# Performance work log

Hardware: AMD Instinct MI355X
Metric: run time of the kernel (lower is better)

The kernel has to match this reference:

```python
import jax, jax.numpy as jnp
import numpy as np

TEMPERATURE = 0.07


def setup_inputs() -> dict:
    key = jax.random.key(0)
    k1, k2 = jax.random.split(key)
    B, D = 4096, 512
    emb1 = jax.random.normal(k1, (B, D), dtype=jnp.float32)
    emb2 = jax.random.normal(k2, (B, D), dtype=jnp.float32)
    # module assumes L2-normalised embeddings
    emb1 = emb1 / jnp.linalg.norm(emb1, axis=-1, keepdims=True)
    emb2 = emb2 / jnp.linalg.norm(emb2, axis=-1, keepdims=True)
    return {"emb1": emb1, "emb2": emb2}


def reference(emb1, emb2):
    B = emb1.shape[0]
    emb = jnp.concatenate([emb1, emb2], axis=0)            # (2B, D)
    sim = jnp.einsum('id,jd->ij', emb, emb) / TEMPERATURE  # (2B, 2B)
    neg_inf = jnp.finfo(sim.dtype).min
    self_mask = jnp.eye(2 * B, dtype=bool)
    sim = jnp.where(self_mask, neg_inf, sim)
    labels = jnp.concatenate([jnp.arange(B, 2 * B), jnp.arange(B)])
    logp = jax.nn.log_softmax(sim, axis=-1)                # stable softmax CE
    nll = -jnp.take_along_axis(logp, labels[:, None], axis=-1)[:, 0]
    return jnp.mean(nll)
```

## Files before the change

kernel.cpp:

```cpp
#include <hip/hip_runtime.h>
#include <hip/hip_bf16.h>

#define B_    4096
#define D_    512
#define TB_   8192
#define BM    128
#define BK    128
#define NK    4
#define NTILE 64
#define NTRI  2080
#define INV_T 14.285714285714286f
#define SCL   (INV_T / 16129.0f)

typedef __attribute__((ext_vector_type(4))) int v4i;

#define GLOAD_LDS16(gp, lp)                                                        \
  __builtin_amdgcn_global_load_lds((const __attribute__((address_space(1))) void*)(gp), \
                                   (__attribute__((address_space(3))) void*)(lp),  \
                                   16, 0, 0)

__global__ void ntx_prep(const float* __restrict__ a, const float* __restrict__ b,
                         char* __restrict__ E8) {
  int t = blockIdx.x * blockDim.x + threadIdx.x;
  int i = t * 16;
  const float* src = (i < B_ * D_) ? (a + i) : (b + (i - B_ * D_));
  v4i o;
#pragma unroll
  for (int g = 0; g < 4; ++g) {
    float4 v = ((const float4*)src)[g];
    int q0 = __float2int_rn(v.x * 127.0f) & 255;
    int q1 = __float2int_rn(v.y * 127.0f) & 255;
    int q2 = __float2int_rn(v.z * 127.0f) & 255;
    int q3 = __float2int_rn(v.w * 127.0f) & 255;
    o[g] = q0 | (q1 << 8) | (q2 << 16) | (q3 << 24);
  }
  ((v4i*)E8)[t] = o;
}

__global__ __launch_bounds__(256, 2)
void ntx_sim(const char* __restrict__ E8, float* __restrict__ P,
             float* __restrict__ pos) {
  __shared__ __align__(16) char As[BM * BK];
  __shared__ __align__(16) char Bs[BM * BK];

  const int bid = blockIdx.x;
  const int t   = (bid & 7) * (NTRI / 8) + (bid >> 3);
  int ti = (int)((129.0f - sqrtf(16641.0f - 8.0f * (float)t)) * 0.5f);
  while (ti * (129 - ti) / 2 > t) --ti;
  while ((ti + 1) * (128 - ti) / 2 <= t) ++ti;
  const int tj = ti + (t - ti * (129 - ti) / 2);
  const int rowTile = ti * BM, colTile = tj * BM;
  const bool diag = (ti == tj);
  const bool posT = (tj == ti + B_ / BM);

  const int tid = threadIdx.x, lane = tid & 63, wave = tid >> 6;
  const int wr = wave >> 1, wc = wave & 1;
  const int llo = lane & 15, lhi = lane >> 4;

  unsigned offA[4], offB[4], ldsOf[4];
#pragma unroll
  for (int r = 0; r < 4; ++r) {
    int ch = r * 256 + tid, row = ch >> 3;
    int sc = ((ch & 7) ^ (row & 7)) << 4;
    offA[r]  = (unsigned)(rowTile + row) * D_ + sc;
    offB[r]  = (unsigned)(colTile + row) * D_ + sc;
    ldsOf[r] = (unsigned)ch * 16;
  }
  unsigned fA[2][4], fB[2][4];
#pragma unroll
  for (int ks = 0; ks < 2; ++ks)
#pragma unroll
    for (int m = 0; m < 4; ++m) {
      int chc = ks * 4 + lhi;
      int ra  = wr * 64 + m * 16 + llo;
      fA[ks][m] = (unsigned)(ra * BK + (((unsigned)chc ^ (ra & 7)) << 4));
      int rb  = wc * 64 + m * 16 + llo;
      fB[ks][m] = (unsigned)(rb * BK + (((unsigned)chc ^ (rb & 7)) << 4));
    }

  v4i acc[4][4] = {};

  for (int kt = 0; kt < NK; ++kt) {
    const unsigned kb = (unsigned)kt * BK;
#pragma unroll
    for (int r = 0; r < 4; ++r) GLOAD_LDS16(E8 + offA[r] + kb, &As[ldsOf[r]]);
#pragma unroll
    for (int r = 0; r < 4; ++r) GLOAD_LDS16(E8 + offB[r] + kb, &Bs[ldsOf[r]]);
    __syncthreads();
#pragma unroll
    for (int ks = 0; ks < 2; ++ks) {
      v4i af[4], bf[4];
#pragma unroll
      for (int m = 0; m < 4; ++m) {
        af[m] = *(const v4i*)&As[fA[ks][m]];
        bf[m] = *(const v4i*)&Bs[fB[ks][m]];
      }
#pragma unroll
      for (int m = 0; m < 4; ++m)
#pragma unroll
        for (int n = 0; n < 4; ++n)
          acc[m][n] = __builtin_amdgcn_mfma_i32_16x16x64_i8(af[m], bf[n],
                                                            acc[m][n], 0, 0, 0);
    }
    __syncthreads();
  }

  float* __restrict__ Prow = P + ((size_t)ti * 2 * NTILE + (size_t)tj * 2 + wc) * BM;
  float* __restrict__ Pcol = P + ((size_t)tj * 2 * NTILE + (size_t)ti * 2 + wr) * BM;
  float cs[4] = {0.f, 0.f, 0.f, 0.f};
#pragma unroll
  for (int m = 0; m < 4; ++m) {
    float rs[4] = {0.f, 0.f, 0.f, 0.f};
#pragma unroll
    for (int n = 0; n < 4; ++n) {
      int gc = colTile + wc * 64 + n * 16 + llo;
#pragma unroll
      for (int jj = 0; jj < 4; ++jj) {
        int gr = rowTile + wr * 64 + m * 16 + lhi * 4 + jj;
        float s = (float)acc[m][n][jj] * SCL;
        if (posT && gc - gr == B_) pos[gr] = s;
        float e = __expf(s);
        e = (diag && gr == gc) ? 0.0f : e;
        rs[jj] += e;
        cs[n]  += e;
      }
    }
#pragma unroll
    for (int jj = 0; jj < 4; ++jj) {
      float v = rs[jj];
      v += __shfl_xor(v, 1);
      v += __shfl_xor(v, 2);
      v += __shfl_xor(v, 4);
      v += __shfl_xor(v, 8);
      if (llo == 0) Prow[wr * 64 + m * 16 + lhi * 4 + jj] = v;
    }
  }
  if (diag) {
    ;
  } else {
#pragma unroll
    for (int n = 0; n < 4; ++n) {
      float v = cs[n];
      v += __shfl_xor(v, 16);
      v += __shfl_xor(v, 32);
      if (lhi == 0) Pcol[wc * 64 + n * 16 + llo] = v;
    }
  }
}

__global__ void ntx_fin1(const float* __restrict__ P, const float* __restrict__ pos,
                         float* __restrict__ par) {
  int r = blockIdx.x * 256 + threadIdx.x;
  int ti = r >> 7, rloc = r & 127;
  const float* base = P + (size_t)ti * 2 * NTILE * BM + rloc;
  float s = 0.f;
#pragma unroll 16
  for (int j = 0; j < 2 * NTILE; ++j) s += base[j * BM];
  float nll = __logf(s) - pos[r & (B_ - 1)];
  float v = nll;
#pragma unroll
  for (int off = 1; off < 64; off <<= 1) v += __shfl_xor(v, off);
  __shared__ float sm[4];
  if ((threadIdx.x & 63) == 0) sm[threadIdx.x >> 6] = v;
  __syncthreads();
  if (threadIdx.x == 0) par[blockIdx.x] = sm[0] + sm[1] + sm[2] + sm[3];
}

__global__ void ntx_fin2(const float* __restrict__ par, float* __restrict__ out) {
  int t = threadIdx.x;
  float s = (t < 32) ? par[t] : 0.f;
#pragma unroll
  for (int off = 1; off < 32; off <<= 1) s += __shfl_xor(s, off);
  if (t == 0) out[0] = s * (1.0f / TB_);
}

extern "C" void kernel_launch(void* const* d_in, const int* in_sizes, int n_in,
                              void* d_out, int out_size, void* d_ws, size_t ws_size,
                              hipStream_t stream) {
  const float* e1 = (const float*)d_in[0];
  const float* e2 = (const float*)d_in[1];
  float* out = (float*)d_out;
  char*  E8  = (char*)d_ws;
  float* P   = (float*)((char*)d_ws + (size_t)TB_ * D_);
  float* pos = P + (size_t)NTILE * 2 * NTILE * BM;
  float* par = pos + B_;

  ntx_prep<<<1024, 256, 0, stream>>>(e1, e2, E8);
  ntx_sim<<<NTRI, 256, 0, stream>>>(E8, P, pos);
  ntx_fin1<<<TB_ / 256, 256, 0, stream>>>(P, pos, par);
  ntx_fin2<<<1, 64, 0, stream>>>(par, out);
}
```

Before: 50.27 us.

## Use 1024-thread blocks with 4x4 waves and LDS-reduced tile partial sums

Grows the similarity kernel from 4 to 16 waves per 128x128 tile, so each wave computes a 32x32 sub-tile and each thread issues one global-to-LDS load per operand per k-step. Row and column exp-sums are reduced across waves in shared memory before a single write per tile, which halves the partial-sum buffer and the number of entries fin1 has to sum. exp is rewritten as exp2 with a prescaled constant. The trade is less register-level data reuse per wave (fewer MFMAs per LDS fragment read), an extra block barrier, and the requirement that 1024-thread blocks can reach the requested occupancy.

After: 58.39 us. 1.16x slower.

```diff
diff --git a/kernel.cpp b/kernel.cpp
--- a/kernel.cpp
+++ b/kernel.cpp
@@ -11,6 +11,7 @@
 #define NTRI  2080
 #define INV_T 14.285714285714286f
 #define SCL   (INV_T / 16129.0f)
+#define SCL2  (SCL * 1.4426950408889634f)
 
 typedef __attribute__((ext_vector_type(4))) int v4i;
 
@@ -37,7 +38,7 @@
   ((v4i*)E8)[t] = o;
 }
 
-__global__ __launch_bounds__(256, 2)
+__global__ __launch_bounds__(1024, 4)
 void ntx_sim(const char* __restrict__ E8, float* __restrict__ P,
              float* __restrict__ pos) {
   __shared__ __align__(16) char As[BM * BK];
@@ -54,72 +55,68 @@
   const bool posT = (tj == ti + B_ / BM);
 
   const int tid = threadIdx.x, lane = tid & 63, wave = tid >> 6;
-  const int wr = wave >> 1, wc = wave & 1;
+  const int wr = wave >> 2;
+  const int wc = wave & 3;
   const int llo = lane & 15, lhi = lane >> 4;
 
-  unsigned offA[4], offB[4], ldsOf[4];
-#pragma unroll
-  for (int r = 0; r < 4; ++r) {
-    int ch = r * 256 + tid, row = ch >> 3;
-    int sc = ((ch & 7) ^ (row & 7)) << 4;
-    offA[r]  = (unsigned)(rowTile + row) * D_ + sc;
-    offB[r]  = (unsigned)(colTile + row) * D_ + sc;
-    ldsOf[r] = (unsigned)ch * 16;
-  }
-  unsigned fA[2][4], fB[2][4];
+  const int ch = tid, srow = ch >> 3;
+  const int sc = ((ch & 7) ^ (srow & 7)) << 4;
+  const unsigned offA  = (unsigned)(rowTile + srow) * D_ + sc;
+  const unsigned offB  = (unsigned)(colTile + srow) * D_ + sc;
+  const unsigned ldsOf = (unsigned)ch * 16;
+
+  unsigned fA[2][2], fB[2][2];
 #pragma unroll
   for (int ks = 0; ks < 2; ++ks)
 #pragma unroll
-    for (int m = 0; m < 4; ++m) {
+    for (int m = 0; m < 2; ++m) {
       int chc = ks * 4 + lhi;
-      int ra  = wr * 64 + m * 16 + llo;
+      int ra  = wr * 32 + m * 16 + llo;
       fA[ks][m] = (unsigned)(ra * BK + (((unsigned)chc ^ (ra & 7)) << 4));
-      int rb  = wc * 64 + m * 16 + llo;
+      int rb  = wc * 32 + m * 16 + llo;
       fB[ks][m] = (unsigned)(rb * BK + (((unsigned)chc ^ (rb & 7)) << 4));
     }
 
-  v4i acc[4][4] = {};
+  v4i acc[2][2] = {};
 
   for (int kt = 0; kt < NK; ++kt) {
     const unsigned kb = (unsigned)kt * BK;
-#pragma unroll
-    for (int r = 0; r < 4; ++r) GLOAD_LDS16(E8 + offA[r] + kb, &As[ldsOf[r]]);
-#pragma unroll
-    for (int r = 0; r < 4; ++r) GLOAD_LDS16(E8 + offB[r] + kb, &Bs[ldsOf[r]]);
+    GLOAD_LDS16(E8 + offA + kb, &As[ldsOf]);
+    GLOAD_LDS16(E8 + offB + kb, &Bs[ldsOf]);
     __syncthreads();
 #pragma unroll
     for (int ks = 0; ks < 2; ++ks) {
-      v4i af[4], bf[4];
+      v4i af[2], bf[2];
 #pragma unroll
-      for (int m = 0; m < 4; ++m) {
+      for (int m = 0; m < 2; ++m) {
         af[m] = *(const v4i*)&As[fA[ks][m]];
         bf[m] = *(const v4i*)&Bs[fB[ks][m]];
       }
 #pragma unroll
-      for (int m = 0; m < 4; ++m)
+      for (int m = 0; m < 2; ++m)
 #pragma unroll
-        for (int n = 0; n < 4; ++n)
+        for (int n = 0; n < 2; ++n)
           acc[m][n] = __builtin_amdgcn_mfma_i32_16x16x64_i8(af[m], bf[n],
                                                             acc[m][n], 0, 0, 0);
     }
     __syncthreads();
   }
 
-  float* __restrict__ Prow = P + ((size_t)ti * 2 * NTILE + (size_t)tj * 2 + wc) * BM;
-  float* __restrict__ Pcol = P + ((size_t)tj * 2 * NTILE + (size_t)ti * 2 + wr) * BM;
-  float cs[4] = {0.f, 0.f, 0.f, 0.f};
+  float* Rbuf = (float*)As;
+  float* Cbuf = (float*)Bs;
+  float cs[2] = {0.f, 0.f};
 #pragma unroll
-  for (int m = 0; m < 4; ++m) {
+  for (int m = 0; m < 2; ++m) {
     float rs[4] = {0.f, 0.f, 0.f, 0.f};
 #pragma unroll
-    for (int n = 0; n < 4; ++n) {
-      int gc = colTile + wc * 64 + n * 16 + llo;
+    for (int n = 0; n < 2; ++n) {
+      int gc = colTile + wc * 32 + n * 16 + llo;
 #pragma unroll
       for (int jj = 0; jj < 4; ++jj) {
-        int gr = rowTile + wr * 64 + m * 16 + lhi * 4 + jj;
-        float s = (float)acc[m][n][jj] * SCL;
-        if (posT && gc - gr == B_) pos[gr] = s;
-        float e = __expf(s);
+        int gr = rowTile + wr * 32 + m * 16 + lhi * 4 + jj;
+        float si = (float)acc[m][n][jj];
+        if (posT && gc - gr == B_) pos[gr] = si * SCL;
+        float e = exp2f(si * SCL2);
         e = (diag && gr == gc) ? 0.0f : e;
         rs[jj] += e;
         cs[n]  += e;
@@ -132,18 +129,25 @@
       v += __shfl_xor(v, 2);
       v += __shfl_xor(v, 4);
       v += __shfl_xor(v, 8);
-      if (llo == 0) Prow[wr * 64 + m * 16 + lhi * 4 + jj] = v;
+      if (llo == 0) Rbuf[wc * 128 + wr * 32 + m * 16 + lhi * 4 + jj] = v;
     }
   }
-  if (diag) {
-    ;
-  } else {
 #pragma unroll
-    for (int n = 0; n < 4; ++n) {
-      float v = cs[n];
-      v += __shfl_xor(v, 16);
-      v += __shfl_xor(v, 32);
-      if (lhi == 0) Pcol[wc * 64 + n * 16 + llo] = v;
+  for (int n = 0; n < 2; ++n) {
+    float v = cs[n];
+    v += __shfl_xor(v, 16);
+    v += __shfl_xor(v, 32);
+    if (lhi == 0) Cbuf[wr * 128 + wc * 32 + n * 16 + llo] = v;
+  }
+  __syncthreads();
+  if (tid < 128) {
+    float v = Rbuf[tid] + Rbuf[128 + tid] + Rbuf[256 + tid] + Rbuf[384 + tid];
+    P[((size_t)ti * NTILE + tj) * BM + tid] = v;
+  } else if (tid < 256) {
+    if (!diag) {
+      int c = tid - 128;
+      float v = Cbuf[c] + Cbuf[128 + c] + Cbuf[256 + c] + Cbuf[384 + c];
+      P[((size_t)tj * NTILE + ti) * BM + c] = v;
     }
   }
 }
@@ -152,10 +156,10 @@
                          float* __restrict__ par) {
   int r = blockIdx.x * 256 + threadIdx.x;
   int ti = r >> 7, rloc = r & 127;
-  const float* base = P + (size_t)ti * 2 * NTILE * BM + rloc;
+  const float* base = P + (size_t)ti * NTILE * BM + rloc;
   float s = 0.f;
 #pragma unroll 16
-  for (int j = 0; j < 2 * NTILE; ++j) s += base[j * BM];
+  for (int j = 0; j < NTILE; ++j) s += base[j * BM];
   float nll = __logf(s) - pos[r & (B_ - 1)];
   float v = nll;
 #pragma unroll
@@ -182,11 +186,11 @@
   float* out = (float*)d_out;
   char*  E8  = (char*)d_ws;
   float* P   = (float*)((char*)d_ws + (size_t)TB_ * D_);
-  float* pos = P + (size_t)NTILE * 2 * NTILE * BM;
+  float* pos = P + (size_t)NTILE * NTILE * BM;
   float* par = pos + B_;
 
   ntx_prep<<<1024, 256, 0, stream>>>(e1, e2, E8);
-  ntx_sim<<<NTRI, 256, 0, stream>>>(E8, P, pos);
+  ntx_sim<<<NTRI, 1024, 0, stream>>>(E8, P, pos);
   ntx_fin1<<<TB_ / 256, 256, 0, stream>>>(P, pos, par);
   ntx_fin2<<<1, 64, 0, stream>>>(par, out);
 }
```

## Enlarge similarity tiles to 256 with 1024-thread blocks and LDS partial-sum reduction

Applied to the files above, without the earlier changes.

Doubles the output tile of the int8 similarity GEMM to 256x256, with 16 waves per block. This halves the global reloads of each embedding row and cuts the number of triangle blocks. Row and column exp-sums are combined across waves in LDS before one write per tile, which shrinks the partial-sum buffer the finisher must scan. Risks: far fewer blocks (528) for load balance, and the launch bound of 1024 threads with 4 blocks may force a very tight VGPR budget and spill the 64-register accumulators.

Result: slower. 55.25 us (+9.9%).

```diff
diff --git a/kernel.cpp b/kernel.cpp
--- a/kernel.cpp
+++ b/kernel.cpp
@@ -4,11 +4,11 @@
 #define B_    4096
 #define D_    512
 #define TB_   8192
-#define BM    128
+#define BM    256
 #define BK    128
 #define NK    4
-#define NTILE 64
-#define NTRI  2080
+#define NT    32
+#define NTRI  528
 #define INV_T 14.285714285714286f
 #define SCL   (INV_T / 16129.0f)
 
@@ -37,7 +37,7 @@
   ((v4i*)E8)[t] = o;
 }
 
-__global__ __launch_bounds__(256, 2)
+__global__ __launch_bounds__(1024, 4)
 void ntx_sim(const char* __restrict__ E8, float* __restrict__ P,
              float* __restrict__ pos) {
   __shared__ __align__(16) char As[BM * BK];
@@ -45,22 +45,23 @@
 
   const int bid = blockIdx.x;
   const int t   = (bid & 7) * (NTRI / 8) + (bid >> 3);
-  int ti = (int)((129.0f - sqrtf(16641.0f - 8.0f * (float)t)) * 0.5f);
-  while (ti * (129 - ti) / 2 > t) --ti;
-  while ((ti + 1) * (128 - ti) / 2 <= t) ++ti;
-  const int tj = ti + (t - ti * (129 - ti) / 2);
+  int ti = (int)((65.0f - sqrtf(4225.0f - 8.0f * (float)t)) * 0.5f);
+  while (ti * (65 - ti) / 2 > t) --ti;
+  while ((ti + 1) * (64 - ti) / 2 <= t) ++ti;
+  const int tj = ti + (t - ti * (65 - ti) / 2);
   const int rowTile = ti * BM, colTile = tj * BM;
   const bool diag = (ti == tj);
   const bool posT = (tj == ti + B_ / BM);
 
   const int tid = threadIdx.x, lane = tid & 63, wave = tid >> 6;
-  const int wr = wave >> 1, wc = wave & 1;
+  const int wr = wave >> 2;
+  const int wc = wave & 3;
   const int llo = lane & 15, lhi = lane >> 4;
 
-  unsigned offA[4], offB[4], ldsOf[4];
+  unsigned offA[2], offB[2], ldsOf[2];
 #pragma unroll
-  for (int r = 0; r < 4; ++r) {
-    int ch = r * 256 + tid, row = ch >> 3;
+  for (int r = 0; r < 2; ++r) {
+    int ch = r * 1024 + tid, row = ch >> 3;
     int sc = ((ch & 7) ^ (row & 7)) << 4;
     offA[r]  = (unsigned)(rowTile + row) * D_ + sc;
     offB[r]  = (unsigned)(colTile + row) * D_ + sc;
@@ -83,9 +84,9 @@
   for (int kt = 0; kt < NK; ++kt) {
     const unsigned kb = (unsigned)kt * BK;
 #pragma unroll
-    for (int r = 0; r < 4; ++r) GLOAD_LDS16(E8 + offA[r] + kb, &As[ldsOf[r]]);
+    for (int r = 0; r < 2; ++r) GLOAD_LDS16(E8 + offA[r] + kb, &As[ldsOf[r]]);
 #pragma unroll
-    for (int r = 0; r < 4; ++r) GLOAD_LDS16(E8 + offB[r] + kb, &Bs[ldsOf[r]]);
+    for (int r = 0; r < 2; ++r) GLOAD_LDS16(E8 + offB[r] + kb, &Bs[ldsOf[r]]);
     __syncthreads();
 #pragma unroll
     for (int ks = 0; ks < 2; ++ks) {
@@ -105,8 +106,8 @@
     __syncthreads();
   }
 
-  float* __restrict__ Prow = P + ((size_t)ti * 2 * NTILE + (size_t)tj * 2 + wc) * BM;
-  float* __restrict__ Pcol = P + ((size_t)tj * 2 * NTILE + (size_t)ti * 2 + wr) * BM;
+  float* Rbuf = (float*)As;
+  float* Cbuf = (float*)Bs;
   float cs[4] = {0.f, 0.f, 0.f, 0.f};
 #pragma unroll
   for (int m = 0; m < 4; ++m) {
@@ -132,30 +133,35 @@
       v += __shfl_xor(v, 2);
       v += __shfl_xor(v, 4);
       v += __shfl_xor(v, 8);
-      if (llo == 0) Prow[wr * 64 + m * 16 + lhi * 4 + jj] = v;
+      if (llo == 0) Rbuf[wc * 256 + wr * 64 + m * 16 + lhi * 4 + jj] = v;
     }
   }
-  if (diag) {
-    ;
-  } else {
 #pragma unroll
-    for (int n = 0; n < 4; ++n) {
-      float v = cs[n];
-      v += __shfl_xor(v, 16);
-      v += __shfl_xor(v, 32);
-      if (lhi == 0) Pcol[wc * 64 + n * 16 + llo] = v;
-    }
+  for (int n = 0; n < 4; ++n) {
+    float v = cs[n];
+    v += __shfl_xor(v, 16);
+    v += __shfl_xor(v, 32);
+    if (lhi == 0) Cbuf[wr * 256 + wc * 64 + n * 16 + llo] = v;
+  }
+  __syncthreads();
+  if (tid < 256) {
+    float v = Rbuf[tid] + Rbuf[256 + tid] + Rbuf[512 + tid] + Rbuf[768 + tid];
+    P[((size_t)ti * NT + tj) * BM + tid] = v;
+  } else if (tid < 512 && !diag) {
+    int c = tid - 256;
+    float v = Cbuf[c] + Cbuf[256 + c] + Cbuf[512 + c] + Cbuf[768 + c];
+    P[((size_t)tj * NT + ti) * BM + c] = v;
   }
 }
 
 __global__ void ntx_fin1(const float* __restrict__ P, const float* __restrict__ pos,
                          float* __restrict__ par) {
   int r = blockIdx.x * 256 + threadIdx.x;
-  int ti = r >> 7, rloc = r & 127;
-  const float* base = P + (size_t)ti * 2 * NTILE * BM + rloc;
+  int ti = r >> 8, rloc = r & 255;
+  const float* base = P + (size_t)ti * NT * BM + rloc;
   float s = 0.f;
-#pragma unroll 16
-  for (int j = 0; j < 2 * NTILE; ++j) s += base[j * BM];
+#pragma unroll 8
+  for (int j = 0; j < NT; ++j) s += base[j * BM];
   float nll = __logf(s) - pos[r & (B_ - 1)];
   float v = nll;
 #pragma unroll
@@ -182,11 +188,11 @@
   float* out = (float*)d_out;
   char*  E8  = (char*)d_ws;
   float* P   = (float*)((char*)d_ws + (size_t)TB_ * D_);
-  float* pos = P + (size_t)NTILE * 2 * NTILE * BM;
+  float* pos = P + (size_t)NT * NT * BM;
   float* par = pos + B_;
 
   ntx_prep<<<1024, 256, 0, stream>>>(e1, e2, E8);
-  ntx_sim<<<NTRI, 256, 0, stream>>>(E8, P, pos);
+  ntx_sim<<<NTRI, 1024, 0, stream>>>(E8, P, pos);
   ntx_fin1<<<TB_ / 256, 256, 0, stream>>>(P, pos, par);
   ntx_fin2<<<1, 64, 0, stream>>>(par, out);
 }
```
